# Performance work log

Measured on AMD Instinct MI355X. Metric: run time of the kernel, lower is better.

The kernel has to match this reference:

```python
import jax, jax.numpy as jnp
import numpy as np

N_NODES = 50000
N_EDGES = 800000
D = 128
N_LAYERS = 4
N_GRAPHS = 512
N_CLASS = 10


def setup_inputs() -> dict:
    key = jax.random.key(0)
    ks = jax.random.split(key, 12)
    x = jax.random.normal(ks[0], (N_NODES, D), dtype=jnp.float32)
    edge_index = jax.random.randint(ks[1], (2, N_EDGES), 0, N_NODES, dtype=jnp.int64)
    batch = jnp.sort(jax.random.randint(ks[2], (N_NODES,), 0, N_GRAPHS, dtype=jnp.int64))
    s = 1.0 / np.sqrt(D)
    W_conv = jax.random.uniform(ks[3], (N_LAYERS, D, D), jnp.float32, -s, s)
    b_conv = jnp.zeros((N_LAYERS, D), jnp.float32)
    W1 = jax.random.uniform(ks[4], (D, D), jnp.float32, -s, s)
    b1 = jnp.zeros((D,), jnp.float32)
    W2 = jax.random.uniform(ks[5], (D, D // 2), jnp.float32, -s, s)
    b2 = jnp.zeros((D // 2,), jnp.float32)
    W3 = jax.random.uniform(ks[6], (D // 2, N_CLASS), jnp.float32, -1.0 / np.sqrt(D // 2), 1.0 / np.sqrt(D // 2))
    b3 = jnp.zeros((N_CLASS,), jnp.float32)
    return {"x": x, "edge_index": edge_index, "batch": batch,
            "W_conv": W_conv, "b_conv": b_conv,
            "W1": W1, "b1": b1, "W2": W2, "b2": b2, "W3": W3, "b3": b3}


def reference(x, edge_index, batch, W_conv, b_conv, W1, b1, W2, b2, W3, b3):
    row, col = edge_index[0], edge_index[1]  # messages: source=row -> target=col
    # GCN symmetric normalization with self-loops (PyG GCNConv default).
    deg = jax.ops.segment_sum(jnp.ones((row.shape[0],), x.dtype), col, num_segments=N_NODES) + 1.0
    dinv = jax.lax.rsqrt(deg)
    edge_norm = (dinv[row] * dinv[col])[:, None]      # [E,1]
    self_norm = (1.0 / deg)[:, None]                  # [N,1] = dinv_i * dinv_i

    def gcn_layer(h, W, b):
        h = h @ W                                      # [N,D]
        agg = jax.ops.segment_sum(h[row] * edge_norm, col, num_segments=N_NODES)
        agg = agg + h * self_norm                      # self-loop contribution
        return jax.nn.relu(agg + b)

    h = x
    for l in range(N_LAYERS):
        h = gcn_layer(h, W_conv[l], b_conv[l])

    # global_add_pool over graph ids
    g = jax.ops.segment_sum(h, batch, num_segments=N_GRAPHS)  # [G,D]

    # MLP head (dropout is identity in eval mode)
    g = jax.nn.relu(g @ W1 + b1)
    g = jax.nn.relu(g @ W2 + b2)
    return g @ W3 + b3
```

## Files before the change

### kernel.cpp

```cpp
#include <hip/hip_runtime.h>
#include <stdint.h>
#include <stddef.h>

#define NN 50000
#define NE 800000
#define DD 128
#define NL 4
#define NG 512
#define NC 10
#define NB 196
#define BCAP 5056
#define GPB 49

using short8 = __attribute__((ext_vector_type(8))) short;
using f32x4  = __attribute__((ext_vector_type(4))) float;

__device__ __forceinline__ float bf2f(unsigned short u) {
  union { unsigned int i; float f; } c; c.i = ((unsigned int)u) << 16; return c.f;
}
__device__ __forceinline__ unsigned short f2bf(float f) {
  union { unsigned int i; float f; } c; c.f = f;
  unsigned int i = c.i;
  return (unsigned short)((i + 0x7FFFu + ((i >> 16) & 1u)) >> 16);
}
__device__ __forceinline__ unsigned int pack2(float a, float b) {
  return (unsigned int)f2bf(a) | ((unsigned int)f2bf(b) << 16);
}
__device__ __forceinline__ void acc8(float* a, uint4 p) {
  a[0] += bf2f((unsigned short)(p.x & 0xffffu)); a[1] += bf2f((unsigned short)(p.x >> 16));
  a[2] += bf2f((unsigned short)(p.y & 0xffffu)); a[3] += bf2f((unsigned short)(p.y >> 16));
  a[4] += bf2f((unsigned short)(p.z & 0xffffu)); a[5] += bf2f((unsigned short)(p.z >> 16));
  a[6] += bf2f((unsigned short)(p.w & 0xffffu)); a[7] += bf2f((unsigned short)(p.w >> 16));
}

__global__ __launch_bounds__(1024) void p1b_k(const int* __restrict__ erow,
                                              const int* __restrict__ ecol,
                                              int* __restrict__ cursor,
                                              unsigned int* __restrict__ ebuf) {
  __shared__ int lcnt[NB], gb[NB];
  int tid = threadIdx.x;
  if (tid < NB) lcnt[tid] = 0;
  __syncthreads();
  int e0 = blockIdx.x * 4096 + tid;
  int bk[4], sl[4]; unsigned int pk[4];
#pragma unroll
  for (int j = 0; j < 4; ++j) {
    int e = e0 + j * 1024;
    bk[j] = -1;
    if (e < NE) {
      int d = ecol[e], s = erow[e];
      bk[j] = d >> 8;
      pk[j] = ((unsigned int)(d & 255) << 16) | (unsigned int)s;
      sl[j] = atomicAdd(&lcnt[bk[j]], 1);
    }
  }
  __syncthreads();
  if (tid < NB) {
    int c = lcnt[tid];
    gb[tid] = c ? atomicAdd(&cursor[tid], c) : 0;
  }
  __syncthreads();
#pragma unroll
  for (int j = 0; j < 4; ++j)
    if (bk[j] >= 0) ebuf[(size_t)bk[j] * BCAP + gb[bk[j]] + sl[j]] = pk[j];
}

__global__ __launch_bounds__(1024) void p2_k(const unsigned int* __restrict__ ebuf,
                                             const int* __restrict__ cursor,
                                             const float* __restrict__ x,
                                             const int* __restrict__ batch,
                                             const float* __restrict__ Wc,
                                             int* __restrict__ csr_ptr,
                                             int* __restrict__ csr_end,
                                             int* __restrict__ csr_src,
                                             float* __restrict__ dinv,
                                             unsigned short* __restrict__ xb,
                                             int* __restrict__ gptr,
                                             unsigned short* __restrict__ Wbt) {
  int b = blockIdx.x, tid = threadIdx.x;
  if (b >= NB + GPB) {
    int l = b - NB - GPB;
    const float* W = Wc + (size_t)l * DD * DD;
    unsigned short* WT = Wbt + (size_t)l * DD * DD;
    for (int i = tid; i < DD * DD; i += 1024) {
      int n = i >> 7, k = i & 127;
      WT[n * DD + k] = f2bf(W[k * DD + n]);
    }
    return;
  }
  if (b >= NB) {
    int i = (b - NB) * 1024 + tid;
    if (i >= NN) return;
    int bb = batch[i];
    int bp = (i == 0) ? -1 : batch[i - 1];
    for (int g = bp + 1; g <= bb; ++g) gptr[g] = i;
    if (i == NN - 1) { for (int g = bb + 1; g <= NG; ++g) gptr[g] = NN; }
    return;
  }

  __shared__ unsigned int pr[BCAP];
  __shared__ int srcb[BCAP];
  __shared__ int hist_s[256], scn[256], lcur[256];
  __shared__ float dinv_s[256];
  size_t beg = (size_t)b * BCAP;
  int cnt = cursor[b];
  if (cnt > BCAP) cnt = BCAP;

  if (tid < 256) hist_s[tid] = 0;
  __syncthreads();
  for (int i = tid; i < cnt; i += 1024) {
    unsigned int p = ebuf[beg + i];
    pr[i] = p;
    atomicAdd(&hist_s[p >> 16], 1);
  }
  __syncthreads();
  if (tid < 256) scn[tid] = hist_s[tid];
  __syncthreads();
  for (int off = 1; off < 256; off <<= 1) {
    int v = (tid < 256 && tid >= off) ? scn[tid - off] : 0;
    __syncthreads();
    if (tid < 256) scn[tid] += v;
    __syncthreads();
  }
  if (tid < 256) {
    int ex = scn[tid] - hist_s[tid];
    lcur[tid] = ex;
    int V = b * 256 + tid;
    if (V < NN) {
      csr_ptr[V] = (int)beg + ex;
      csr_end[V] = (int)beg + scn[tid];
      float dv = rsqrtf((float)(hist_s[tid] + 1));
      dinv[V] = dv;
      dinv_s[tid] = dv;
    }
  }
  __syncthreads();
  for (int i = tid; i < cnt; i += 1024) {
    unsigned int p = pr[i];
    int pos = atomicAdd(&lcur[p >> 16], 1);
    srcb[pos] = (int)(p & 0xFFFFu);
  }
  __syncthreads();
  for (int i = tid; i < cnt; i += 1024) csr_src[beg + i] = srcb[i];

  for (int i4 = tid; i4 < 256 * 32; i4 += 1024) {
    int vl = i4 >> 5;
    int V = b * 256 + vl;
    if (V < NN) {
      float d = dinv_s[vl];
      int q = i4 & 31;
      f32x4 vx = *((const f32x4*)(x + (size_t)V * DD) + q);
      uint2 o;
      o.x = pack2(vx[0] * d, vx[1] * d);
      o.y = pack2(vx[2] * d, vx[3] * d);
      ((uint2*)(xb + (size_t)V * DD))[q] = o;
    }
  }
}

__global__ __launch_bounds__(1024, 8) void flayer_k(
    const unsigned short* __restrict__ hs,
    const unsigned short* __restrict__ Wb,
    const float* __restrict__ bias,
    unsigned short* __restrict__ out,
    const float* __restrict__ dscale,
    const int* __restrict__ csr_ptr,
    const int* __restrict__ csr_end,
    const int* __restrict__ csr_src,
    const float* __restrict__ dinv) {
  __shared__ unsigned short Wt[128][136];
  __shared__ unsigned short At[16][136];

  int tid = threadIdx.x;
  for (int i = tid; i < 128 * 16; i += 1024) {
    int rr = i >> 4, c = i & 15;
    *(uint4*)&Wt[rr][c * 8] = *(const uint4*)(Wb + rr * DD + c * 8);
  }

  int wave = tid >> 6, lane = tid & 63;
  int qg = lane >> 4, r = lane & 15;
  int v = blockIdx.x * 16 + wave;
  const uint4* rows = (const uint4*)hs;

  float a[8] = {0.f, 0.f, 0.f, 0.f, 0.f, 0.f, 0.f, 0.f};
  float b[8] = {0.f, 0.f, 0.f, 0.f, 0.f, 0.f, 0.f, 0.f};
  if (qg == 0) acc8(a, rows[(size_t)v * 16 + r]);

  int e = csr_ptr[v] + qg, end = csr_end[v];
  for (; e + 12 < end; e += 16) {
    int s0 = csr_src[e];
    int s1 = csr_src[e + 4];
    int s2 = csr_src[e + 8];
    int s3 = csr_src[e + 12];
    uint4 p0 = rows[(size_t)s0 * 16 + r];
    uint4 p1 = rows[(size_t)s1 * 16 + r];
    uint4 p2 = rows[(size_t)s2 * 16 + r];
    uint4 p3 = rows[(size_t)s3 * 16 + r];
    acc8(a, p0); acc8(b, p1); acc8(a, p2); acc8(b, p3);
  }
  for (; e + 4 < end; e += 8) {
    int s0 = csr_src[e];
    int s1 = csr_src[e + 4];
    uint4 p0 = rows[(size_t)s0 * 16 + r];
    uint4 p1 = rows[(size_t)s1 * 16 + r];
    acc8(a, p0); acc8(b, p1);
  }
  if (e < end) acc8(a, rows[(size_t)csr_src[e] * 16 + r]);

#pragma unroll
  for (int t = 0; t < 8; ++t) a[t] += b[t];
#pragma unroll
  for (int t = 0; t < 8; ++t) {
    a[t] += __shfl_xor(a[t], 16, 64);
    a[t] += __shfl_xor(a[t], 32, 64);
  }

  if (qg == 0) {
    float dv = dinv[v];
    uint4 o;
    o.x = pack2(dv * a[0], dv * a[1]);
    o.y = pack2(dv * a[2], dv * a[3]);
    o.z = pack2(dv * a[4], dv * a[5]);
    o.w = pack2(dv * a[6], dv * a[7]);
    *(uint4*)&At[wave][r * 8] = o;
  }
  __syncthreads();

  if (wave < 8) {
    short8 afrag[4];
#pragma unroll
    for (int ks = 0; ks < 4; ++ks)
      afrag[ks] = *(const short8*)&At[r][ks * 32 + qg * 8];

    f32x4 acc = (f32x4){0.f, 0.f, 0.f, 0.f};
#pragma unroll
    for (int ks = 0; ks < 4; ++ks) {
      short8 bfrag = *(const short8*)(&Wt[wave * 16 + r][ks * 32 + qg * 8]);
      acc = __builtin_amdgcn_mfma_f32_16x16x32_bf16(afrag[ks], bfrag, acc, 0, 0, 0);
    }

    int orow = blockIdx.x * 16 + qg * 4;
    int coln = wave * 16 + r;
    float bc = bias[coln];
#pragma unroll
    for (int reg = 0; reg < 4; ++reg) {
      int rr = orow + reg;
      float sc = dscale ? dscale[rr] : 1.f;
      float val = fmaxf(acc[reg] + bc, 0.f) * sc;
      out[(size_t)rr * DD + coln] = f2bf(val);
    }
  }
}

__global__ __launch_bounds__(128) void poolmlp_k(const unsigned short* __restrict__ h,
                                                 const int* __restrict__ gptr,
                                                 const float* __restrict__ W1,
                                                 const float* __restrict__ b1,
                                                 const float* __restrict__ W2,
                                                 const float* __restrict__ b2,
                                                 const float* __restrict__ W3,
                                                 const float* __restrict__ b3,
                                                 float* __restrict__ out) {
  __shared__ float s_g[128], s_h1[128], s_h2[64];
  int g = blockIdx.x, t = threadIdx.x;
  int beg = gptr[g], end = gptr[g + 1];
  float acc = 0.f;
  for (int v = beg; v < end; ++v) acc += bf2f(h[(size_t)v * DD + t]);
  s_g[t] = acc;
  __syncthreads();
  {
    float a = b1[t];
    for (int k = 0; k < 128; ++k) a += s_g[k] * W1[k * 128 + t];
    s_h1[t] = fmaxf(a, 0.f);
  }
  __syncthreads();
  if (t < 64) {
    float a = b2[t];
    for (int k = 0; k < 128; ++k) a += s_h1[k] * W2[k * 64 + t];
    s_h2[t] = fmaxf(a, 0.f);
  }
  __syncthreads();
  if (t < NC) {
    float a = b3[t];
    for (int k = 0; k < 64; ++k) a += s_h2[k] * W3[k * NC + t];
    out[g * NC + t] = a;
  }
}


extern "C" void kernel_launch(void* const* d_in, const int* in_sizes, int n_in,
                              void* d_out, int out_size, void* d_ws, size_t ws_size,
                              hipStream_t stream) {
  const float* x     = (const float*)d_in[0];
  const int*   ei    = (const int*)d_in[1];
  const int*   batch = (const int*)d_in[2];
  const float* Wc    = (const float*)d_in[3];
  const float* bc    = (const float*)d_in[4];
  const float* W1    = (const float*)d_in[5];
  const float* b1    = (const float*)d_in[6];
  const float* W2    = (const float*)d_in[7];
  const float* b2    = (const float*)d_in[8];
  const float* W3    = (const float*)d_in[9];
  const float* b3    = (const float*)d_in[10];
  float* out = (float*)d_out;

  const int* erow = ei;
  const int* ecol = ei + NE;

  char* w = (char*)d_ws;
  int*   cursor  = (int*)w;    w += NB * 4;
  int*   csr_ptr = (int*)w;    w += (size_t)(NN + 4) * 4;
  int*   csr_end = (int*)w;    w += (size_t)(NN + 4) * 4;
  int*   gptr    = (int*)w;    w += (NG + 4) * 4;
  int*   csr_src = (int*)w;    w += (size_t)NB * BCAP * 4;
  float* dinv    = (float*)w;  w += (size_t)NN * 4;
  w = (char*)(((uintptr_t)w + 255) & ~(uintptr_t)255);
  unsigned short* Wbt  = (unsigned short*)w; w += (size_t)NL * DD * DD * 2;
  unsigned short* xb   = (unsigned short*)w; w += (size_t)NN * DD * 2;
  unsigned short* hA   = (unsigned short*)w; w += (size_t)NN * DD * 2;
  unsigned short* hB   = (unsigned short*)w; w += (size_t)NN * DD * 2;
  unsigned int* ebuf = (unsigned int*)hA;

  hipMemsetAsync(cursor, 0, NB * 4, stream);

  p1b_k<<<NB, 1024, 0, stream>>>(erow, ecol, cursor, ebuf);
  p2_k <<<NB + GPB + NL, 1024, 0, stream>>>(ebuf, cursor, x, batch, Wc, csr_ptr,
                                            csr_end, csr_src, dinv, xb, gptr, Wbt);

  const int fGrid = NN / 16;

  for (int l = 0; l < NL; ++l) {
    const unsigned short* hin = (l == 0) ? xb : ((l & 1) ? hA : hB);
    unsigned short* dst = (l & 1) ? hB : hA;
    const float* dsc = (l == NL - 1) ? nullptr : dinv;
    flayer_k<<<fGrid, 1024, 0, stream>>>(hin, Wbt + (size_t)l * DD * DD,
                                         bc + (size_t)l * DD, dst, dsc,
                                         csr_ptr, csr_end, csr_src, dinv);
  }

  poolmlp_k<<<NG, 128, 0, stream>>>(hB, gptr, W1, b1, W2, b2, W3, b3, out);

  (void)in_sizes; (void)n_in; (void)out_size; (void)ws_size;
}
```

Baseline: 329.1 us.

## Process two destination nodes per wave and 32 rows per block in fused GCN layer

Each wave now gathers neighbour rows for two destination nodes at once, interleaving their loads so more independent memory requests are in flight. Each block covers 32 nodes, and all 16 waves join the MFMA transform instead of only 8. This also halves the number of blocks and the per-block reload of the 128x128 weight tile into LDS. In exchange it adds register pressure, imbalance when the two nodes have different degrees, and bounds checks for the ragged last block.

```diff
diff --git a/kernel.cpp b/kernel.cpp
--- a/kernel.cpp
+++ b/kernel.cpp
@@ -31,6 +31,30 @@
   a[2] += bf2f((unsigned short)(p.y & 0xffffu)); a[3] += bf2f((unsigned short)(p.y >> 16));
   a[4] += bf2f((unsigned short)(p.z & 0xffffu)); a[5] += bf2f((unsigned short)(p.z >> 16));
   a[6] += bf2f((unsigned short)(p.w & 0xffffu)); a[7] += bf2f((unsigned short)(p.w >> 16));
+}
+
+__device__ __forceinline__ void drain_row(const uint4* __restrict__ rows,
+                                          const int* __restrict__ csr_src,
+                                          int e, int end, int r, float* A) {
+  for (; e + 12 < end; e += 16) {
+    int s0 = csr_src[e];
+    int s1 = csr_src[e + 4];
+    int s2 = csr_src[e + 8];
+    int s3 = csr_src[e + 12];
+    uint4 p0 = rows[(size_t)s0 * 16 + r];
+    uint4 p1 = rows[(size_t)s1 * 16 + r];
+    uint4 p2 = rows[(size_t)s2 * 16 + r];
+    uint4 p3 = rows[(size_t)s3 * 16 + r];
+    acc8(A, p0); acc8(A, p1); acc8(A, p2); acc8(A, p3);
+  }
+  for (; e + 4 < end; e += 8) {
+    int s0 = csr_src[e];
+    int s1 = csr_src[e + 4];
+    uint4 p0 = rows[(size_t)s0 * 16 + r];
+    uint4 p1 = rows[(size_t)s1 * 16 + r];
+    acc8(A, p0); acc8(A, p1);
+  }
+  if (e < end) acc8(A, rows[(size_t)csr_src[e] * 16 + r]);
 }
 
 __global__ __launch_bounds__(1024) void p1b_k(const int* __restrict__ erow,
@@ -169,7 +193,7 @@
     const int* __restrict__ csr_src,
     const float* __restrict__ dinv) {
   __shared__ unsigned short Wt[128][136];
-  __shared__ unsigned short At[16][136];
+  __shared__ unsigned short At[32][136];
 
   int tid = threadIdx.x;
   for (int i = tid; i < 128 * 16; i += 1024) {
@@ -179,75 +203,95 @@
 
   int wave = tid >> 6, lane = tid & 63;
   int qg = lane >> 4, r = lane & 15;
-  int v = blockIdx.x * 16 + wave;
+  int row0 = blockIdx.x * 32;
+  int v0 = row0 + wave * 2, v1 = v0 + 1;
+  bool ok0 = v0 < NN, ok1 = v1 < NN;
   const uint4* rows = (const uint4*)hs;
 
-  float a[8] = {0.f, 0.f, 0.f, 0.f, 0.f, 0.f, 0.f, 0.f};
-  float b[8] = {0.f, 0.f, 0.f, 0.f, 0.f, 0.f, 0.f, 0.f};
-  if (qg == 0) acc8(a, rows[(size_t)v * 16 + r]);
-
-  int e = csr_ptr[v] + qg, end = csr_end[v];
-  for (; e + 12 < end; e += 16) {
-    int s0 = csr_src[e];
-    int s1 = csr_src[e + 4];
-    int s2 = csr_src[e + 8];
-    int s3 = csr_src[e + 12];
-    uint4 p0 = rows[(size_t)s0 * 16 + r];
-    uint4 p1 = rows[(size_t)s1 * 16 + r];
-    uint4 p2 = rows[(size_t)s2 * 16 + r];
-    uint4 p3 = rows[(size_t)s3 * 16 + r];
-    acc8(a, p0); acc8(b, p1); acc8(a, p2); acc8(b, p3);
-  }
-  for (; e + 4 < end; e += 8) {
-    int s0 = csr_src[e];
-    int s1 = csr_src[e + 4];
-    uint4 p0 = rows[(size_t)s0 * 16 + r];
-    uint4 p1 = rows[(size_t)s1 * 16 + r];
-    acc8(a, p0); acc8(b, p1);
-  }
-  if (e < end) acc8(a, rows[(size_t)csr_src[e] * 16 + r]);
-
-#pragma unroll
-  for (int t = 0; t < 8; ++t) a[t] += b[t];
+  float A0[8] = {0.f, 0.f, 0.f, 0.f, 0.f, 0.f, 0.f, 0.f};
+  float A1[8] = {0.f, 0.f, 0.f, 0.f, 0.f, 0.f, 0.f, 0.f};
+  if (qg == 0) {
+    if (ok0) acc8(A0, rows[(size_t)v0 * 16 + r]);
+    if (ok1) acc8(A1, rows[(size_t)v1 * 16 + r]);
+  }
+
+  int e0 = 0, end0 = 0, e1 = 0, end1 = 0;
+  if (ok0) { e0 = csr_ptr[v0] + qg; end0 = csr_end[v0]; }
+  if (ok1) { e1 = csr_ptr[v1] + qg; end1 = csr_end[v1]; }
+
+  while (e0 + 12 < end0 && e1 + 12 < end1) {
+    int s00 = csr_src[e0], s01 = csr_src[e0 + 4], s02 = csr_src[e0 + 8], s03 = csr_src[e0 + 12];
+    int s10 = csr_src[e1], s11 = csr_src[e1 + 4], s12 = csr_src[e1 + 8], s13 = csr_src[e1 + 12];
+    uint4 p00 = rows[(size_t)s00 * 16 + r];
+    uint4 p10 = rows[(size_t)s10 * 16 + r];
+    uint4 p01 = rows[(size_t)s01 * 16 + r];
+    uint4 p11 = rows[(size_t)s11 * 16 + r];
+    uint4 p02 = rows[(size_t)s02 * 16 + r];
+    uint4 p12 = rows[(size_t)s12 * 16 + r];
+    uint4 p03 = rows[(size_t)s03 * 16 + r];
+    uint4 p13 = rows[(size_t)s13 * 16 + r];
+    acc8(A0, p00); acc8(A1, p10); acc8(A0, p01); acc8(A1, p11);
+    acc8(A0, p02); acc8(A1, p12); acc8(A0, p03); acc8(A1, p13);
+    e0 += 16; e1 += 16;
+  }
+  drain_row(rows, csr_src, e0, end0, r, A0);
+  drain_row(rows, csr_src, e1, end1, r, A1);
+
 #pragma unroll
   for (int t = 0; t < 8; ++t) {
-    a[t] += __shfl_xor(a[t], 16, 64);
-    a[t] += __shfl_xor(a[t], 32, 64);
+    A0[t] += __shfl_xor(A0[t], 16, 64);
+    A0[t] += __shfl_xor(A0[t], 32, 64);
+    A1[t] += __shfl_xor(A1[t], 16, 64);
+    A1[t] += __shfl_xor(A1[t], 32, 64);
   }
 
   if (qg == 0) {
-    float dv = dinv[v];
     uint4 o;
-    o.x = pack2(dv * a[0], dv * a[1]);
-    o.y = pack2(dv * a[2], dv * a[3]);
-    o.z = pack2(dv * a[4], dv * a[5]);
-    o.w = pack2(dv * a[6], dv * a[7]);
-    *(uint4*)&At[wave][r * 8] = o;
-  }
-  __syncthreads();
-
-  if (wave < 8) {
+    if (ok0) {
+      float dv = dinv[v0];
+      o.x = pack2(dv * A0[0], dv * A0[1]);
+      o.y = pack2(dv * A0[2], dv * A0[3]);
+      o.z = pack2(dv * A0[4], dv * A0[5]);
+      o.w = pack2(dv * A0[6], dv * A0[7]);
+    } else { o.x = 0u; o.y = 0u; o.z = 0u; o.w = 0u; }
+    *(uint4*)&At[wave * 2][r * 8] = o;
+    if (ok1) {
+      float dv = dinv[v1];
+      o.x = pack2(dv * A1[0], dv * A1[1]);
+      o.y = pack2(dv * A1[2], dv * A1[3]);
+      o.z = pack2(dv * A1[4], dv * A1[5]);
+      o.w = pack2(dv * A1[6], dv * A1[7]);
+    } else { o.x = 0u; o.y = 0u; o.z = 0u; o.w = 0u; }
+    *(uint4*)&At[wave * 2 + 1][r * 8] = o;
+  }
+  __syncthreads();
+
+  {
+    int rg = wave >> 3, cg = wave & 7;
+
     short8 afrag[4];
 #pragma unroll
     for (int ks = 0; ks < 4; ++ks)
-      afrag[ks] = *(const short8*)&At[r][ks * 32 + qg * 8];
+      afrag[ks] = *(const short8*)&At[rg * 16 + r][ks * 32 + qg * 8];
 
     f32x4 acc = (f32x4){0.f, 0.f, 0.f, 0.f};
 #pragma unroll
     for (int ks = 0; ks < 4; ++ks) {
-      short8 bfrag = *(const short8*)(&Wt[wave * 16 + r][ks * 32 + qg * 8]);
+      short8 bfrag = *(const short8*)(&Wt[cg * 16 + r][ks * 32 + qg * 8]);
       acc = __builtin_amdgcn_mfma_f32_16x16x32_bf16(afrag[ks], bfrag, acc, 0, 0, 0);
     }
 
-    int orow = blockIdx.x * 16 + qg * 4;
-    int coln = wave * 16 + r;
+    int orow = row0 + rg * 16 + qg * 4;
+    int coln = cg * 16 + r;
     float bc = bias[coln];
 #pragma unroll
     for (int reg = 0; reg < 4; ++reg) {
       int rr = orow + reg;
-      float sc = dscale ? dscale[rr] : 1.f;
-      float val = fmaxf(acc[reg] + bc, 0.f) * sc;
-      out[(size_t)rr * DD + coln] = f2bf(val);
+      if (rr < NN) {
+        float sc = dscale ? dscale[rr] : 1.f;
+        float val = fmaxf(acc[reg] + bc, 0.f) * sc;
+        out[(size_t)rr * DD + coln] = f2bf(val);
+      }
     }
   }
 }
@@ -327,7 +371,7 @@
   p2_k <<<NB + GPB + NL, 1024, 0, stream>>>(ebuf, cursor, x, batch, Wc, csr_ptr,
                                             csr_end, csr_src, dinv, xb, gptr, Wbt);
 
-  const int fGrid = NN / 16;
+  const int fGrid = (NN + 31) / 32;
 
   for (int l = 0; l < NL; ++l) {
     const unsigned short* hin = (l == 0) ? xb : ((l & 1) ? hA : hB);
```

Result: slower. 361.1 us (+9.7%).
